# Kernel tuning notes

Hardware: AMD Instinct MI355X
Metric: run time of the kernel (lower is better)

## Reference

```python
import jax, jax.numpy as jnp
import numpy as np

N = 100000   # nodes
E = 1600000  # edges (avg degree 16)
D = 256      # in_channels == dim (forward hard-codes BatchNorm1d(256))
BN_EPS = 1e-5


def _batchnorm(x, gamma, beta):
    # training-mode BatchNorm1d: batch statistics over node dim, biased variance
    mu = jnp.mean(x, axis=0)
    var = jnp.var(x, axis=0)
    return (x - mu) * jax.lax.rsqrt(var + BN_EPS) * gamma + beta


def _gin_conv(x, src, dst, n, W1, b1, gamma, beta, W2, b2):
    # GINConv, eps=0: nn((1+eps)*x + sum_{j in N(i)} x_j)
    agg = jax.ops.segment_sum(x[src], dst, num_segments=n)  # sparse neighbor sum
    h = x + agg
    h = jax.nn.relu(_batchnorm(h @ W1 + b1, gamma, beta))
    return jax.nn.relu(h @ W2 + b2)


def setup_inputs() -> dict:
    key = jax.random.key(0)
    ks = jax.random.split(key, 8)
    x = jax.random.normal(ks[0], (N, D), dtype=jnp.float32)
    edge_index = jax.random.randint(ks[1], (2, E), 0, N, dtype=jnp.int64)
    s = 0.02
    inp = {
        "x": x,
        "edge_index": edge_index,
        # fresh BatchNorm1d(256) in forward (default affine params)
        "g0": jnp.ones((D,), jnp.float32),
        "b0": jnp.zeros((D,), jnp.float32),
        # conv1 MLP: Linear-BN-ReLU-Linear-ReLU
        "W1a": jax.random.normal(ks[2], (D, D), jnp.float32) * s,
        "b1a": jnp.zeros((D,), jnp.float32),
        "g1": jnp.ones((D,), jnp.float32),
        "bt1": jnp.zeros((D,), jnp.float32),
        "W1b": jax.random.normal(ks[3], (D, D), jnp.float32) * s,
        "b1b": jnp.zeros((D,), jnp.float32),
        # conv2 MLP
        "W2a": jax.random.normal(ks[4], (D, D), jnp.float32) * s,
        "b2a": jnp.zeros((D,), jnp.float32),
        "g2": jnp.ones((D,), jnp.float32),
        "bt2": jnp.zeros((D,), jnp.float32),
        "W2b": jax.random.normal(ks[5], (D, D), jnp.float32) * s,
        "b2b": jnp.zeros((D,), jnp.float32),
    }
    return inp


def reference(x, edge_index, g0, b0, W1a, b1a, g1, bt1, W1b, b1b,
              W2a, b2a, g2, bt2, W2b, b2b):
    n = x.shape[0]
    src, dst = edge_index[0], edge_index[1]
    h = _batchnorm(x, g0, b0)                       # fresh BN(256) on input
    h = _gin_conv(h, src, dst, n, W1a, b1a, g1, bt1, W1b, b1b)
    h = jax.nn.relu(h)                              # outer relu (dropout=eval, identity)
    h = _gin_conv(h, src, dst, n, W2a, b2a, g2, bt2, W2b, b2b)
    return jax.nn.relu(h)
```

## Files before the change

kernel.cpp:

```cpp
#include <hip/hip_runtime.h>

#define N_NODES 100000
#define N_EDGES 1600000
#define DIM 256

typedef unsigned short bf16u;
typedef __attribute__((ext_vector_type(8))) short bf16x8s;
typedef __attribute__((ext_vector_type(4))) float f32x4;

__device__ __forceinline__ float bf2f(unsigned int u16) {
    union { unsigned int i; float f; } x; x.i = u16 << 16; return x.f;
}
__device__ __forceinline__ bf16u f2bf(float f) {
    union { float f; unsigned int i; } x; x.f = f;
    unsigned int i = x.i;
    return (bf16u)((i + 0x7fffu + ((i >> 16) & 1u)) >> 16);
}
__device__ __forceinline__ float loadv(const void* p, size_t i, int isf32) {
    return isf32 ? ((const float*)p)[i] : bf2f(((const bf16u*)p)[i]);
}
__device__ __forceinline__ void async_copy16(const void* g, void* l) {
    __builtin_amdgcn_global_load_lds((const __attribute__((address_space(1))) void*)g,
                                     (__attribute__((address_space(3))) void*)l, 16, 0, 0);
}

__global__ void zero_ints(int* p, int n) {
    int i = blockIdx.x * 256 + threadIdx.x;
    if (i < n) p[i] = 0;
}
__global__ void zero_floats(float* p, int n) {
    int i = blockIdx.x * 256 + threadIdx.x;
    if (i < n) p[i] = 0.f;
}

__global__ void detect_flags(const unsigned* xw, const int* ei, int* flags) {
    __shared__ int cnt, nz;
    if (threadIdx.x == 0) { cnt = 0; nz = 0; }
    __syncthreads();
    unsigned u = xw[threadIdx.x];
    float av = fabsf(bf2f(u & 0xffffu));
    if (av > 1e-5f && av < 50.f) atomicAdd(&cnt, 1);
    if (ei[2 * threadIdx.x + 1] != 0) atomicAdd(&nz, 1);
    __syncthreads();
    if (threadIdx.x == 0) {
        flags[0] = (cnt >= 128) ? 0 : 1;
        if (nz == 0) { flags[1] = 2; flags[2] = 2 * N_EDGES; }
        else         { flags[1] = 1; flags[2] = N_EDGES; }
    }
}

__global__ void transpose_w(const void* W0, const void* W1, const void* W2, const void* W3,
                            bf16u* Wt, const int* flags) {
    __shared__ bf16u tile[64][65];
    int isf32 = flags[0];
    const void* W = (blockIdx.y == 0) ? W0 : (blockIdx.y == 1) ? W1 : (blockIdx.y == 2) ? W2 : W3;
    bf16u* out = Wt + (size_t)blockIdx.y * DIM * DIM;
    int t = threadIdx.x;
    int tx = t & 63, ty = t >> 6;
    int k0 = (blockIdx.x >> 2) * 64, n0 = (blockIdx.x & 3) * 64;
#pragma unroll
    for (int i = 0; i < 16; ++i) {
        int r = ty + i * 4;
        tile[tx][r] = f2bf(loadv(W, (size_t)(k0 + r) * DIM + (n0 + tx), isf32));
    }
    __syncthreads();
#pragma unroll
    for (int i = 0; i < 16; ++i) {
        int r = ty + i * 4;
        out[(size_t)(n0 + r) * DIM + (k0 + tx)] = tile[r][tx];
    }
}

__global__ void col_stats(const void* X, int nrows, float* sums, const int* flags, int dual) {
    __shared__ float ls[512];
    int isf32 = dual ? flags[0] : 0;
    int t = threadIdx.x;
    ls[t] = 0.f; ls[t + 256] = 0.f;
    __syncthreads();
    int rpb = (nrows + gridDim.x - 1) / gridDim.x;
    int r0 = blockIdx.x * rpb;
    int r1 = r0 + rpb; if (r1 > nrows) r1 = nrows;
    int cg = (t & 31) * 8;
    float s[8], q[8];
#pragma unroll
    for (int j = 0; j < 8; ++j) { s[j] = 0.f; q[j] = 0.f; }
    for (int r = r0 + (t >> 5); r < r1; r += 8) {
        size_t base = (size_t)r * DIM + cg;
#pragma unroll
        for (int j = 0; j < 8; ++j) {
            float f = loadv(X, base + j, isf32);
            s[j] += f; q[j] += f * f;
        }
    }
#pragma unroll
    for (int j = 0; j < 8; ++j) {
        atomicAdd(&ls[cg + j], s[j]);
        atomicAdd(&ls[256 + cg + j], q[j]);
    }
    __syncthreads();
    atomicAdd(&sums[t], ls[t]);
    atomicAdd(&sums[256 + t], ls[256 + t]);
}

__global__ void bn_finalize(const float* sums, const void* gamma, const void* beta,
                            float* sc, float* sh, float inv_n, const int* flags) {
    int isf32 = flags[0];
    int t = threadIdx.x;
    float mu = sums[t] * inv_n;
    float var = sums[256 + t] * inv_n - mu * mu;
    float rs = rsqrtf(var + 1e-5f);
    float g = loadv(gamma, t, isf32), b = loadv(beta, t, isf32);
    sc[t] = rs * g;
    sh[t] = b - mu * rs * g;
}

__global__ void bn_apply(const void* X, const float* sc, const float* sh, bf16u* Y,
                         const int* flags, int dual, int relu) {
    int isf32 = dual ? flags[0] : 0;
    size_t i = (size_t)blockIdx.x * 256 + threadIdx.x;
    int c = ((int)(i & 31)) * 8;
    size_t base = i * 8;
    float v[8];
    if (isf32) {
        f32x4 x0 = *(const f32x4*)((const float*)X + base);
        f32x4 x1 = *(const f32x4*)((const float*)X + base + 4);
#pragma unroll
        for (int j = 0; j < 4; ++j) { v[j] = x0[j]; v[4 + j] = x1[j]; }
    } else {
        uint4 u = *(const uint4*)((const bf16u*)X + base);
        v[0] = bf2f(u.x & 0xffffu); v[1] = bf2f(u.x >> 16);
        v[2] = bf2f(u.y & 0xffffu); v[3] = bf2f(u.y >> 16);
        v[4] = bf2f(u.z & 0xffffu); v[5] = bf2f(u.z >> 16);
        v[6] = bf2f(u.w & 0xffffu); v[7] = bf2f(u.w >> 16);
    }
    f32x4 s0 = *(const f32x4*)(sc + c), s1 = *(const f32x4*)(sc + c + 4);
    f32x4 h0 = *(const f32x4*)(sh + c), h1 = *(const f32x4*)(sh + c + 4);
    float y[8];
#pragma unroll
    for (int j = 0; j < 4; ++j) {
        y[j]     = v[j]     * s0[j] + h0[j];
        y[4 + j] = v[4 + j] * s1[j] + h1[j];
    }
    if (relu) {
#pragma unroll
        for (int j = 0; j < 8; ++j) y[j] = fmaxf(y[j], 0.f);
    }
    uint4 ov;
    ov.x = (unsigned)f2bf(y[0]) | ((unsigned)f2bf(y[1]) << 16);
    ov.y = (unsigned)f2bf(y[2]) | ((unsigned)f2bf(y[3]) << 16);
    ov.z = (unsigned)f2bf(y[4]) | ((unsigned)f2bf(y[5]) << 16);
    ov.w = (unsigned)f2bf(y[6]) | ((unsigned)f2bf(y[7]) << 16);
    *(uint4*)(Y + base) = ov;
}

__global__ void edge_hist(const int* ei, const int* flags, int* deg) {
    int e = blockIdx.x * 256 + threadIdx.x;
    if (e < N_EDGES) atomicAdd(&deg[ei[(size_t)flags[2] + (size_t)e * flags[1]]], 1);
}

__global__ void scan1(const int* deg, int* rp, int* bsum) {
    __shared__ int s[256];
    int t = threadIdx.x;
    int i = blockIdx.x * 256 + t;
    s[t] = (i < N_NODES) ? deg[i] : 0;
    __syncthreads();
    for (int off = 1; off < 256; off <<= 1) {
        int nv = (t >= off) ? s[t - off] : 0;
        __syncthreads();
        s[t] += nv;
        __syncthreads();
    }
    if (i < N_NODES) rp[i + 1] = s[t];
    if (t == 255) bsum[blockIdx.x] = s[255];
}

__global__ void scan2(int* bsum, int nblocks) {
    __shared__ int s[512];
    int t = threadIdx.x;
    s[t] = (t < nblocks) ? bsum[t] : 0;
    __syncthreads();
    for (int off = 1; off < 512; off <<= 1) {
        int nv = (t >= off) ? s[t - off] : 0;
        __syncthreads();
        s[t] += nv;
        __syncthreads();
    }
    if (t < nblocks) bsum[t] = s[t];
}

__global__ void scan3(int* rp, const int* bsum) {
    int i = blockIdx.x * 256 + threadIdx.x;
    if (i == 0) rp[0] = 0;
    if (i < N_NODES) {
        int b = i >> 8;
        if (b > 0) rp[i + 1] += bsum[b - 1];
    }
}

__global__ void csr_fill(const int* ei, const int* flags, const int* rp, int* fill, int* col) {
    int e = blockIdx.x * 256 + threadIdx.x;
    if (e < N_EDGES) {
        int d = ei[(size_t)flags[2] + (size_t)e * flags[1]];
        int s = ei[(size_t)e * flags[1]];
        int p = rp[d] + atomicAdd(&fill[d], 1);
        col[p] = s;
    }
}

__global__ void aggregate(const bf16u* h, const int* rp, const int* col, bf16u* out) {
    int node = blockIdx.x * 4 + (threadIdx.x >> 6);
    int lane = threadIdx.x & 63;
    const uint2* hv = (const uint2*)h;
    uint2 u = hv[(size_t)node * 64 + lane];
    float a0 = bf2f(u.x & 0xffffu), a1 = bf2f(u.x >> 16);
    float a2 = bf2f(u.y & 0xffffu), a3 = bf2f(u.y >> 16);
    float b0 = 0.f, b1 = 0.f, b2 = 0.f, b3 = 0.f;
    float c0 = 0.f, c1 = 0.f, c2 = 0.f, c3 = 0.f;
    float d0 = 0.f, d1 = 0.f, d2 = 0.f, d3 = 0.f;
    int e = rp[node], e1 = rp[node + 1];
    for (; e + 4 <= e1; e += 4) {
        int s0 = col[e], s1 = col[e + 1], s2 = col[e + 2], s3 = col[e + 3];
        uint2 w0 = hv[(size_t)s0 * 64 + lane];
        uint2 w1 = hv[(size_t)s1 * 64 + lane];
        uint2 w2 = hv[(size_t)s2 * 64 + lane];
        uint2 w3 = hv[(size_t)s3 * 64 + lane];
        a0 += bf2f(w0.x & 0xffffu); a1 += bf2f(w0.x >> 16); a2 += bf2f(w0.y & 0xffffu); a3 += bf2f(w0.y >> 16);
        b0 += bf2f(w1.x & 0xffffu); b1 += bf2f(w1.x >> 16); b2 += bf2f(w1.y & 0xffffu); b3 += bf2f(w1.y >> 16);
        c0 += bf2f(w2.x & 0xffffu); c1 += bf2f(w2.x >> 16); c2 += bf2f(w2.y & 0xffffu); c3 += bf2f(w2.y >> 16);
        d0 += bf2f(w3.x & 0xffffu); d1 += bf2f(w3.x >> 16); d2 += bf2f(w3.y & 0xffffu); d3 += bf2f(w3.y >> 16);
    }
    for (; e < e1; ++e) {
        uint2 w0 = hv[(size_t)col[e] * 64 + lane];
        a0 += bf2f(w0.x & 0xffffu); a1 += bf2f(w0.x >> 16); a2 += bf2f(w0.y & 0xffffu); a3 += bf2f(w0.y >> 16);
    }
    a0 += b0 + (c0 + d0); a1 += b1 + (c1 + d1);
    a2 += b2 + (c2 + d2); a3 += b3 + (c3 + d3);
    uint2 ov;
    ov.x = (unsigned)f2bf(a0) | ((unsigned)f2bf(a1) << 16);
    ov.y = (unsigned)f2bf(a2) | ((unsigned)f2bf(a3) << 16);
    *(uint2*)&((uint2*)out)[(size_t)node * 64 + lane] = ov;
}

__global__ __launch_bounds__(256) void gemm_bias(const bf16u* __restrict__ A,
                                                 const bf16u* __restrict__ Wt,
                                                 const void* __restrict__ bias,
                                                 void* __restrict__ Cout, int mrows,
                                                 const int* __restrict__ flags,
                                                 int relu, int f32out,
                                                 float* __restrict__ stats) {
    __shared__ bf16u As[128 * 64];
    __shared__ bf16u Bs[128 * 64];
    __shared__ float lsum[256];
    int isf32 = flags[0];
    int t = threadIdx.x;
    int w = t >> 6, lane = t & 63;
    int lr = lane & 15, lq = lane >> 4;
    int wm = w >> 1, wn = w & 1;
    int rowBase = blockIdx.x * 128, colBase = blockIdx.y * 128;
    f32x4 acc[4][4] = {};
    lsum[t] = 0.f;
    int srow = t >> 3;
    int g8   = ((t & 7) ^ ((t >> 3) & 7)) * 8;
    for (int k0 = 0; k0 < 256; k0 += 64) {
        __syncthreads();
#pragma unroll
        for (int p = 0; p < 4; ++p) {
            int r = p * 32 + srow;
            int gr = rowBase + r; gr = (gr < mrows) ? gr : (mrows - 1);
            async_copy16(A + (size_t)gr * 256 + k0 + g8, &As[(p * 32 + (w << 3)) * 64]);
            async_copy16(Wt + (size_t)(colBase + r) * 256 + k0 + g8, &Bs[(p * 32 + (w << 3)) * 64]);
        }
        __syncthreads();
#pragma unroll
        for (int ks = 0; ks < 2; ++ks) {
            bf16x8s af[4], bfv[4];
#pragma unroll
            for (int mt = 0; mt < 4; ++mt) {
                int ar = wm * 64 + mt * 16 + lr;
                af[mt] = *(const bf16x8s*)&As[ar * 64 + (((ks * 4 + lq) ^ (lr & 7)) * 8)];
            }
#pragma unroll
            for (int nt = 0; nt < 4; ++nt) {
                int br = wn * 64 + nt * 16 + lr;
                bfv[nt] = *(const bf16x8s*)&Bs[br * 64 + (((ks * 4 + lq) ^ (lr & 7)) * 8)];
            }
#pragma unroll
            for (int mt = 0; mt < 4; ++mt)
#pragma unroll
                for (int nt = 0; nt < 4; ++nt)
                    acc[mt][nt] = __builtin_amdgcn_mfma_f32_16x16x32_bf16(af[mt], bfv[nt], acc[mt][nt], 0, 0, 0);
        }
    }
    int storef32 = f32out && isf32;
#pragma unroll
    for (int nt = 0; nt < 4; ++nt) {
        int cl = wn * 64 + nt * 16 + lr;
        int c = colBase + cl;
        float bv = loadv(bias, c, isf32);
        float ssum = 0.f, ssq = 0.f;
#pragma unroll
        for (int mt = 0; mt < 4; ++mt) {
            int r0 = rowBase + wm * 64 + mt * 16 + lq * 4;
#pragma unroll
            for (int j = 0; j < 4; ++j) {
                int r = r0 + j;
                if (r < mrows) {
                    float y = acc[mt][nt][j] + bv;
                    if (relu) y = fmaxf(y, 0.f);
                    if (storef32) ((float*)Cout)[(size_t)r * 256 + c] = y;
                    else          ((bf16u*)Cout)[(size_t)r * 256 + c] = f2bf(y);
                    ssum += y; ssq += y * y;
                }
            }
        }
        if (stats) {
            atomicAdd(&lsum[cl], ssum);
            atomicAdd(&lsum[128 + cl], ssq);
        }
    }
    if (stats) {
        __syncthreads();
        if (t < 128) {
            atomicAdd(&stats[colBase + t], lsum[t]);
            atomicAdd(&stats[256 + colBase + t], lsum[128 + t]);
        }
    }
}

extern "C" void kernel_launch(void* const* d_in, const int* in_sizes, int n_in,
                              void* d_out, int out_size, void* d_ws, size_t ws_size,
                              hipStream_t stream) {
    const void* x   = d_in[0];
    const int*  ei  = (const int*)d_in[1];
    const void* g0  = d_in[2];
    const void* b0  = d_in[3];
    const void* W1a = d_in[4];
    const void* b1a = d_in[5];
    const void* g1  = d_in[6];
    const void* bt1 = d_in[7];
    const void* W1b = d_in[8];
    const void* b1b = d_in[9];
    const void* W2a = d_in[10];
    const void* b2a = d_in[11];
    const void* g2  = d_in[12];
    const void* bt2 = d_in[13];
    const void* W2b = d_in[14];
    const void* b2b = d_in[15];

    char* ws = (char*)d_ws;
    size_t off = 0;
    auto alloc = [&](size_t bytes) {
        char* p = ws + off;
        off += (bytes + 255) & ~(size_t)255;
        return p;
    };
    const size_t FB = (size_t)N_NODES * DIM * 2;
    bf16u* bufA  = (bf16u*)alloc(FB);
    bf16u* bufB  = (bf16u*)alloc(FB);
    bf16u* Wt    = (bf16u*)alloc((size_t)4 * DIM * DIM * 2);
    int*   colA  = (int*)alloc((size_t)N_EDGES * 4);
    int*   rp    = (int*)alloc((size_t)(N_NODES + 1) * 4);
    int*   deg   = (int*)alloc((size_t)N_NODES * 4);
    int*   fill  = (int*)alloc((size_t)N_NODES * 4);
    int*   bsum  = (int*)alloc(512 * 4);
    float* sums0 = (float*)alloc(512 * 4);
    float* sums1 = (float*)alloc(512 * 4);
    float* sums2 = (float*)alloc(512 * 4);
    float* sc    = (float*)alloc(256 * 4);
    float* sh    = (float*)alloc(256 * 4);
    int*   flags = (int*)alloc(4 * 4);

    bf16u* Wt1a = Wt;
    bf16u* Wt1b = Wt + 65536;
    bf16u* Wt2a = Wt + 2 * 65536;
    bf16u* Wt2b = Wt + 3 * 65536;

    const float inv_n = 1.0f / (float)N_NODES;

    detect_flags<<<1, 256, 0, stream>>>((const unsigned*)x, ei, flags);
    zero_floats<<<6, 256, 0, stream>>>(sums0, 1536);
    transpose_w<<<dim3(16, 4), 256, 0, stream>>>(W1a, W1b, W2a, W2b, Wt, flags);

    zero_ints<<<391, 256, 0, stream>>>(deg, N_NODES);
    zero_ints<<<391, 256, 0, stream>>>(fill, N_NODES);
    edge_hist<<<6250, 256, 0, stream>>>(ei, flags, deg);
    scan1<<<391, 256, 0, stream>>>(deg, rp, bsum);
    scan2<<<1, 512, 0, stream>>>(bsum, 391);
    scan3<<<392, 256, 0, stream>>>(rp, bsum);
    csr_fill<<<6250, 256, 0, stream>>>(ei, flags, rp, fill, colA);

    col_stats<<<500, 256, 0, stream>>>(x, N_NODES, sums0, flags, 1);
    bn_finalize<<<1, 256, 0, stream>>>(sums0, g0, b0, sc, sh, inv_n, flags);
    bn_apply<<<12500, 256, 0, stream>>>(x, sc, sh, bufB, flags, 1, 0);

    aggregate<<<25000, 256, 0, stream>>>(bufB, rp, colA, bufA);
    gemm_bias<<<dim3(782, 2), 256, 0, stream>>>(bufA, Wt1a, b1a, bufB, N_NODES, flags, 0, 0, sums1);
    bn_finalize<<<1, 256, 0, stream>>>(sums1, g1, bt1, sc, sh, inv_n, flags);
    bn_apply<<<12500, 256, 0, stream>>>(bufB, sc, sh, bufB, flags, 0, 1);
    gemm_bias<<<dim3(782, 2), 256, 0, stream>>>(bufB, Wt1b, b1b, bufA, N_NODES, flags, 1, 0, nullptr);

    aggregate<<<25000, 256, 0, stream>>>(bufA, rp, colA, bufB);
    gemm_bias<<<dim3(782, 2), 256, 0, stream>>>(bufB, Wt2a, b2a, bufA, N_NODES, flags, 0, 0, sums2);
    bn_finalize<<<1, 256, 0, stream>>>(sums2, g2, bt2, sc, sh, inv_n, flags);
    bn_apply<<<12500, 256, 0, stream>>>(bufA, sc, sh, bufA, flags, 0, 1);
    gemm_bias<<<dim3(782, 2), 256, 0, stream>>>(bufA, Wt2b, b2b, d_out, N_NODES, flags, 1, 1, nullptr);
}
```

Before: 967.5 us.

## Keep full weight matrix in LDS for 128x256 GEMM tiles; widen aggregate unroll

The GEMM now runs one 512-thread block per 128-row strip covering all 256 output columns. The whole 256x256 bf16 weight is staged once into swizzled LDS, and A fragments are read directly from global memory instead of being staged through LDS. This removes the duplicate A reads across two column blocks and the per-k-step barriers, at the cost of 128KB of LDS per block, which limits occupancy. The aggregate kernel gathers eight neighbors per iteration with eight accumulator sets to expose more memory-level parallelism, which raises register use.

After: 1.042 ms. +7.7%, slower.

```diff
diff --git a/kernel.cpp b/kernel.cpp
--- a/kernel.cpp
+++ b/kernel.cpp
@@ -18,10 +18,6 @@
 }
 __device__ __forceinline__ float loadv(const void* p, size_t i, int isf32) {
     return isf32 ? ((const float*)p)[i] : bf2f(((const bf16u*)p)[i]);
-}
-__device__ __forceinline__ void async_copy16(const void* g, void* l) {
-    __builtin_amdgcn_global_load_lds((const __attribute__((address_space(1))) void*)g,
-                                     (__attribute__((address_space(3))) void*)l, 16, 0, 0);
 }
 
 __global__ void zero_ints(int* p, int n) {
@@ -212,90 +208,102 @@
     int lane = threadIdx.x & 63;
     const uint2* hv = (const uint2*)h;
     uint2 u = hv[(size_t)node * 64 + lane];
-    float a0 = bf2f(u.x & 0xffffu), a1 = bf2f(u.x >> 16);
-    float a2 = bf2f(u.y & 0xffffu), a3 = bf2f(u.y >> 16);
-    float b0 = 0.f, b1 = 0.f, b2 = 0.f, b3 = 0.f;
-    float c0 = 0.f, c1 = 0.f, c2 = 0.f, c3 = 0.f;
-    float d0 = 0.f, d1 = 0.f, d2 = 0.f, d3 = 0.f;
+    float ax[8], ay[8], az[8], aw[8];
+#pragma unroll
+    for (int j = 0; j < 8; ++j) { ax[j] = 0.f; ay[j] = 0.f; az[j] = 0.f; aw[j] = 0.f; }
+    ax[0] = bf2f(u.x & 0xffffu); ay[0] = bf2f(u.x >> 16);
+    az[0] = bf2f(u.y & 0xffffu); aw[0] = bf2f(u.y >> 16);
     int e = rp[node], e1 = rp[node + 1];
+    for (; e + 8 <= e1; e += 8) {
+        uint2 w[8];
+#pragma unroll
+        for (int j = 0; j < 8; ++j) w[j] = hv[(size_t)col[e + j] * 64 + lane];
+#pragma unroll
+        for (int j = 0; j < 8; ++j) {
+            ax[j] += bf2f(w[j].x & 0xffffu); ay[j] += bf2f(w[j].x >> 16);
+            az[j] += bf2f(w[j].y & 0xffffu); aw[j] += bf2f(w[j].y >> 16);
+        }
+    }
     for (; e + 4 <= e1; e += 4) {
-        int s0 = col[e], s1 = col[e + 1], s2 = col[e + 2], s3 = col[e + 3];
-        uint2 w0 = hv[(size_t)s0 * 64 + lane];
-        uint2 w1 = hv[(size_t)s1 * 64 + lane];
-        uint2 w2 = hv[(size_t)s2 * 64 + lane];
-        uint2 w3 = hv[(size_t)s3 * 64 + lane];
-        a0 += bf2f(w0.x & 0xffffu); a1 += bf2f(w0.x >> 16); a2 += bf2f(w0.y & 0xffffu); a3 += bf2f(w0.y >> 16);
-        b0 += bf2f(w1.x & 0xffffu); b1 += bf2f(w1.x >> 16); b2 += bf2f(w1.y & 0xffffu); b3 += bf2f(w1.y >> 16);
-        c0 += bf2f(w2.x & 0xffffu); c1 += bf2f(w2.x >> 16); c2 += bf2f(w2.y & 0xffffu); c3 += bf2f(w2.y >> 16);
-        d0 += bf2f(w3.x & 0xffffu); d1 += bf2f(w3.x >> 16); d2 += bf2f(w3.y & 0xffffu); d3 += bf2f(w3.y >> 16);
+        uint2 w[4];
+#pragma unroll
+        for (int j = 0; j < 4; ++j) w[j] = hv[(size_t)col[e + j] * 64 + lane];
+#pragma unroll
+        for (int j = 0; j < 4; ++j) {
+            ax[j] += bf2f(w[j].x & 0xffffu); ay[j] += bf2f(w[j].x >> 16);
+            az[j] += bf2f(w[j].y & 0xffffu); aw[j] += bf2f(w[j].y >> 16);
+        }
     }
     for (; e < e1; ++e) {
+        int j = e & 7;
         uint2 w0 = hv[(size_t)col[e] * 64 + lane];
-        a0 += bf2f(w0.x & 0xffffu); a1 += bf2f(w0.x >> 16); a2 += bf2f(w0.y & 0xffffu); a3 += bf2f(w0.y >> 16);
-    }
-    a0 += b0 + (c0 + d0); a1 += b1 + (c1 + d1);
-    a2 += b2 + (c2 + d2); a3 += b3 + (c3 + d3);
+        ax[j] += bf2f(w0.x & 0xffffu); ay[j] += bf2f(w0.x >> 16);
+        az[j] += bf2f(w0.y & 0xffffu); aw[j] += bf2f(w0.y >> 16);
+    }
+    float r0 = ((ax[0] + ax[1]) + (ax[2] + ax[3])) + ((ax[4] + ax[5]) + (ax[6] + ax[7]));
+    float r1 = ((ay[0] + ay[1]) + (ay[2] + ay[3])) + ((ay[4] + ay[5]) + (ay[6] + ay[7]));
+    float r2 = ((az[0] + az[1]) + (az[2] + az[3])) + ((az[4] + az[5]) + (az[6] + az[7]));
+    float r3 = ((aw[0] + aw[1]) + (aw[2] + aw[3])) + ((aw[4] + aw[5]) + (aw[6] + aw[7]));
     uint2 ov;
-    ov.x = (unsigned)f2bf(a0) | ((unsigned)f2bf(a1) << 16);
-    ov.y = (unsigned)f2bf(a2) | ((unsigned)f2bf(a3) << 16);
-    *(uint2*)&((uint2*)out)[(size_t)node * 64 + lane] = ov;
-}
-
-__global__ __launch_bounds__(256) void gemm_bias(const bf16u* __restrict__ A,
-                                                 const bf16u* __restrict__ Wt,
-                                                 const void* __restrict__ bias,
-                                                 void* __restrict__ Cout, int mrows,
-                                                 const int* __restrict__ flags,
-                                                 int relu, int f32out,
-                                                 float* __restrict__ stats) {
-    __shared__ bf16u As[128 * 64];
-    __shared__ bf16u Bs[128 * 64];
-    __shared__ float lsum[256];
+    ov.x = (unsigned)f2bf(r0) | ((unsigned)f2bf(r1) << 16);
+    ov.y = (unsigned)f2bf(r2) | ((unsigned)f2bf(r3) << 16);
+    ((uint2*)out)[(size_t)node * 64 + lane] = ov;
+}
+
+__global__ __launch_bounds__(512, 2) void gemm_fused(const bf16u* __restrict__ A,
+                                                     const bf16u* __restrict__ Wt,
+                                                     const void* __restrict__ bias,
+                                                     void* __restrict__ Cout, int mrows,
+                                                     const int* __restrict__ flags,
+                                                     int relu, int f32out,
+                                                     float* __restrict__ stats) {
+    __shared__ bf16u Bs[256 * 256];
+    __shared__ float lsum[512];
     int isf32 = flags[0];
     int t = threadIdx.x;
+#pragma unroll
+    for (int i = 0; i < 16; ++i) {
+        int idx = i * 512 + t;
+        int n = idx >> 5, c = idx & 31;
+        bf16x8s v = *(const bf16x8s*)(Wt + n * 256 + c * 8);
+        *(bf16x8s*)&Bs[n * 256 + ((c ^ (n & 7)) * 8)] = v;
+    }
+    lsum[t < 512 ? t : 0] = 0.f;
+    __syncthreads();
+
     int w = t >> 6, lane = t & 63;
     int lr = lane & 15, lq = lane >> 4;
-    int wm = w >> 1, wn = w & 1;
-    int rowBase = blockIdx.x * 128, colBase = blockIdx.y * 128;
+    int wm = w & 1, wn = w >> 1;
+    int rowBase = blockIdx.x * 128;
+    const bf16u* aptr[4];
+#pragma unroll
+    for (int mt = 0; mt < 4; ++mt) {
+        int gr = rowBase + wm * 64 + mt * 16 + lr;
+        gr = (gr < mrows) ? gr : (mrows - 1);
+        aptr[mt] = A + (size_t)gr * 256 + lq * 8;
+    }
     f32x4 acc[4][4] = {};
-    lsum[t] = 0.f;
-    int srow = t >> 3;
-    int g8   = ((t & 7) ^ ((t >> 3) & 7)) * 8;
-    for (int k0 = 0; k0 < 256; k0 += 64) {
-        __syncthreads();
-#pragma unroll
-        for (int p = 0; p < 4; ++p) {
-            int r = p * 32 + srow;
-            int gr = rowBase + r; gr = (gr < mrows) ? gr : (mrows - 1);
-            async_copy16(A + (size_t)gr * 256 + k0 + g8, &As[(p * 32 + (w << 3)) * 64]);
-            async_copy16(Wt + (size_t)(colBase + r) * 256 + k0 + g8, &Bs[(p * 32 + (w << 3)) * 64]);
-        }
-        __syncthreads();
-#pragma unroll
-        for (int ks = 0; ks < 2; ++ks) {
-            bf16x8s af[4], bfv[4];
-#pragma unroll
-            for (int mt = 0; mt < 4; ++mt) {
-                int ar = wm * 64 + mt * 16 + lr;
-                af[mt] = *(const bf16x8s*)&As[ar * 64 + (((ks * 4 + lq) ^ (lr & 7)) * 8)];
-            }
-#pragma unroll
-            for (int nt = 0; nt < 4; ++nt) {
-                int br = wn * 64 + nt * 16 + lr;
-                bfv[nt] = *(const bf16x8s*)&Bs[br * 64 + (((ks * 4 + lq) ^ (lr & 7)) * 8)];
-            }
-#pragma unroll
-            for (int mt = 0; mt < 4; ++mt)
-#pragma unroll
-                for (int nt = 0; nt < 4; ++nt)
-                    acc[mt][nt] = __builtin_amdgcn_mfma_f32_16x16x32_bf16(af[mt], bfv[nt], acc[mt][nt], 0, 0, 0);
-        }
+#pragma unroll
+    for (int ks = 0; ks < 8; ++ks) {
+        bf16x8s af[4], bfv[4];
+#pragma unroll
+        for (int mt = 0; mt < 4; ++mt)
+            af[mt] = *(const bf16x8s*)(aptr[mt] + ks * 32);
+#pragma unroll
+        for (int nt = 0; nt < 4; ++nt) {
+            int br = wn * 64 + nt * 16 + lr;
+            bfv[nt] = *(const bf16x8s*)&Bs[br * 256 + (((ks * 4 + lq) ^ (lr & 7)) * 8)];
+        }
+#pragma unroll
+        for (int mt = 0; mt < 4; ++mt)
+#pragma unroll
+            for (int nt = 0; nt < 4; ++nt)
+                acc[mt][nt] = __builtin_amdgcn_mfma_f32_16x16x32_bf16(af[mt], bfv[nt], acc[mt][nt], 0, 0, 0);
     }
     int storef32 = f32out && isf32;
 #pragma unroll
     for (int nt = 0; nt < 4; ++nt) {
-        int cl = wn * 64 + nt * 16 + lr;
-        int c = colBase + cl;
+        int c = wn * 64 + nt * 16 + lr;
         float bv = loadv(bias, c, isf32);
         float ssum = 0.f, ssq = 0.f;
 #pragma unroll
@@ -314,16 +322,13 @@
             }
         }
         if (stats) {
-            atomicAdd(&lsum[cl], ssum);
-            atomicAdd(&lsum[128 + cl], ssq);
+            atomicAdd(&lsum[c], ssum);
+            atomicAdd(&lsum[256 + c], ssq);
         }
     }
     if (stats) {
         __syncthreads();
-        if (t < 128) {
-            atomicAdd(&stats[colBase + t], lsum[t]);
-            atomicAdd(&stats[256 + colBase + t], lsum[128 + t]);
-        }
+        atomicAdd(&stats[t], lsum[t]);
     }
 }
 
@@ -394,14 +399,14 @@
     bn_apply<<<12500, 256, 0, stream>>>(x, sc, sh, bufB, flags, 1, 0);
 
     aggregate<<<25000, 256, 0, stream>>>(bufB, rp, colA, bufA);
-    gemm_bias<<<dim3(782, 2), 256, 0, stream>>>(bufA, Wt1a, b1a, bufB, N_NODES, flags, 0, 0, sums1);
+    gemm_fused<<<782, 512, 0, stream>>>(bufA, Wt1a, b1a, bufB, N_NODES, flags, 0, 0, sums1);
     bn_finalize<<<1, 256, 0, stream>>>(sums1, g1, bt1, sc, sh, inv_n, flags);
     bn_apply<<<12500, 256, 0, stream>>>(bufB, sc, sh, bufB, flags, 0, 1);
-    gemm_bias<<<dim3(782, 2), 256, 0, stream>>>(bufB, Wt1b, b1b, bufA, N_NODES, flags, 1, 0, nullptr);
+    gemm_fused<<<782, 512, 0, stream>>>(bufB, Wt1b, b1b, bufA, N_NODES, flags, 1, 0, nullptr);
 
     aggregate<<<25000, 256, 0, stream>>>(bufA, rp, colA, bufB);
-    gemm_bias<<<dim3(782, 2), 256, 0, stream>>>(bufB, Wt2a, b2a, bufA, N_NODES, flags, 0, 0, sums2);
+    gemm_fused<<<782, 512, 0, stream>>>(bufB, Wt2a, b2a, bufA, N_NODES, flags, 0, 0, sums2);
     bn_finalize<<<1, 256, 0, stream>>>(sums2, g2, bt2, sc, sh, inv_n, flags);
     bn_apply<<<12500, 256, 0, stream>>>(bufA, sc, sh, bufA, flags, 0, 1);
-    gemm_bias<<<dim3(782, 2), 256, 0, stream>>>(bufA, Wt2b, b2b, d_out, N_NODES, flags, 1, 1, nullptr);
-}
+    gemm_fused<<<782, 512, 0, stream>>>(bufA, Wt2b, b2b, d_out, N_NODES, flags, 1, 1, nullptr);
+}
```
